# Performance work log

Hardware: AMD Instinct MI355X
Metric: run time of the kernel (lower is better)

## Reference

```python
import jax, jax.numpy as jnp
import numpy as np

L, N, E, D, H = 3, 20000, 320000, 128, 4
EPS = 1.1920929e-07  # torch RMSNorm default eps = finfo(float32).eps
NEG_SLOPE = 0.2      # PyG GATConv leaky_relu negative_slope


def rmsnorm(x, w):
    return x * jax.lax.rsqrt(jnp.mean(x * x, axis=-1, keepdims=True) + EPS) * w


def setup_inputs() -> dict:
    key = jax.random.key(0)
    ks = jax.random.split(key, 13)
    s = 0.02
    x = jax.random.normal(ks[0], (N, D), jnp.float32)
    src = jax.random.randint(ks[1], (E,), 0, N, dtype=jnp.int64)
    dst = jax.random.randint(ks[2], (E,), 0, N, dtype=jnp.int64)
    dst = jnp.where(dst == src, (dst + 1) % N, dst)  # no pre-existing self loops
    edge_index = jnp.stack([src, dst])
    return {
        "x": x,
        "W_gat": jax.random.normal(ks[3], (L, D, H * D), jnp.float32) * s,
        "att_src": jax.random.normal(ks[4], (L, H, D), jnp.float32) * s,
        "att_dst": jax.random.normal(ks[5], (L, H, D), jnp.float32) * s,
        "bias_gat": jax.random.normal(ks[6], (L, D), jnp.float32) * s,
        "W1": jax.random.normal(ks[7], (L, D, D), jnp.float32) * s,
        "b1": jax.random.normal(ks[8], (L, D), jnp.float32) * s,
        "W2": jax.random.normal(ks[9], (L, D, D), jnp.float32) * s,
        "b2": jax.random.normal(ks[10], (L, D), jnp.float32) * s,
        "norm1_w": jnp.ones((L, D), jnp.float32),
        "norm2_w": jnp.ones((L, D), jnp.float32),
        "edge_index": edge_index,
    }


def reference(x, W_gat, att_src, att_dst, bias_gat, W1, b1, W2, b2, norm1_w, norm2_w, edge_index):
    # PyG GATConv adds self loops by default
    loops = jnp.arange(N, dtype=edge_index.dtype)
    src = jnp.concatenate([edge_index[0], loops])  # [E+N]
    dst = jnp.concatenate([edge_index[1], loops])
    for i in range(L):
        # --- GATConv(hidden, hidden, heads=H, concat=False), dropout=0 (eval) ---
        xp = (x @ W_gat[i]).reshape(N, H, D)               # [N,H,D]
        a_s = jnp.einsum('nhd,hd->nh', xp, att_src[i])     # [N,H]
        a_d = jnp.einsum('nhd,hd->nh', xp, att_dst[i])
        e = jax.nn.leaky_relu(a_s[src] + a_d[dst], NEG_SLOPE)  # [E+N,H]
        m = jax.ops.segment_max(e, dst, num_segments=N)
        ex = jnp.exp(e - m[dst])
        denom = jax.ops.segment_sum(ex, dst, num_segments=N)
        alpha = ex / denom[dst]                             # segment softmax over incoming edges
        agg = jax.ops.segment_sum(alpha[:, :, None] * xp[src], dst, num_segments=N)  # [N,H,D]
        x_att = agg.mean(axis=1) + bias_gat[i]              # concat=False -> head mean, then bias
        # --- residual + RMSNorm ---
        x = rmsnorm(x + x_att, norm1_w[i])
        # --- FFN ---
        h = jax.nn.relu(x @ W1[i] + b1[i])
        h = h @ W2[i] + b2[i]
        x = rmsnorm(x + h, norm2_w[i])
    return x
```

## Files before the change

### kernel.cpp

```cpp
#include <hip/hip_runtime.h>
#include <hip/hip_bf16.h>

#define N_NODES 20000
#define NEDGE   320000
#define DIM     128
#define NH      4
#define HD      512
#define LAYERS  3
#define EPS_RMS 1.1920929e-07f
#define SLOPE   0.2f
#define NTILES  (N_NODES >> 4)

#define NWGC  (LAYERS * DIM * HD)
#define NW1C  (LAYERS * DIM * DIM)
#define NVC   (LAYERS * DIM)
#define NPACK (NWGC + 2 * NW1C + 5 * NVC)
#define NXV   (N_NODES * DIM / 8)

typedef __bf16 bf16_t;
typedef __bf16 bf16v2 __attribute__((ext_vector_type(2)));
typedef __bf16 bf16v8 __attribute__((ext_vector_type(8)));
typedef float  f32v4  __attribute__((ext_vector_type(4)));
typedef float  f32v2  __attribute__((ext_vector_type(2)));

__device__ __forceinline__ int clamp_node(int s) {
    return ((unsigned)s >= (unsigned)N_NODES) ? 0 : s;
}
__device__ __forceinline__ float leaky(float e) { return e > 0.f ? e : SLOPE * e; }
__device__ __forceinline__ unsigned char enc_fp8(float v) {
    int p = __builtin_amdgcn_cvt_pk_fp8_f32(v, v, 0, false);
    return (unsigned char)(p & 0xff);
}
__device__ __forceinline__ unsigned short enc_fp8_pair(float a, float b) {
    int p = __builtin_amdgcn_cvt_pk_fp8_f32(a, b, 0, false);
    return (unsigned short)(p & 0xffff);
}

__device__ __forceinline__ bool wave_detect_bf16(const unsigned short* xh) {
    int lane = threadIdx.x & 63;
    unsigned short hw = xh[2 * lane];
    int e = (hw >> 7) & 0xff;
    unsigned long long b = __ballot(e >= 96 && e <= 140);
    return __popcll(b) >= 48;
}
__device__ __forceinline__ bool wave_detect_i64(const int* ei) {
    int lane = threadIdx.x & 63;
    unsigned long long b = __ballot(ei[2 * lane + 1] != 0);
    return b == 0ULL;
}
__device__ __forceinline__ float raw_elem(const void* in, size_t j, bool isbf) {
    return isbf ? (float)((const bf16_t*)in)[j] : ((const float*)in)[j];
}
__device__ __forceinline__ bf16_t cvt_elem(const void* in, size_t j, bool isbf) {
    return isbf ? ((const bf16_t*)in)[j] : (bf16_t)((const float*)in)[j];
}
__device__ __forceinline__ int edge_src(const int* ei, int e, bool is64) {
    return clamp_node(is64 ? ei[2 * e] : ei[e]);
}
__device__ __forceinline__ int edge_dst(const int* ei, int e, bool is64) {
    return clamp_node(is64 ? ei[2 * NEDGE + 2 * e] : ei[NEDGE + e]);
}

__global__ __launch_bounds__(256) void prep_v(const void* x, const void* Wg,
                                              const void* aS, const void* aD,
                                              float* __restrict__ vS, float* __restrict__ vD,
                                              int* __restrict__ deg) {
    int gid = blockIdx.x * 256 + threadIdx.x;
    for (int i = gid; i < N_NODES; i += gridDim.x * 256) deg[i] = 0;
    bool isbf = wave_detect_bf16((const unsigned short*)x);
    int w = gid >> 6;
    if (w >= LAYERS * DIM * NH * 2) return;
    int lane = threadIdx.x & 63;
    int sd = w & 1, h = (w >> 1) & 3, k = (w >> 3) & 127, l = w >> 10;
    const void* att = sd ? aD : aS;
    size_t wbase = (size_t)l * DIM * HD + (size_t)k * HD + h * DIM;
    size_t abase = (size_t)l * NH * DIM + (size_t)h * DIM;
    int c = 2 * lane;
    float p = raw_elem(Wg, wbase + c, isbf) * raw_elem(att, abase + c, isbf)
            + raw_elem(Wg, wbase + c + 1, isbf) * raw_elem(att, abase + c + 1, isbf);
#pragma unroll
    for (int msk = 1; msk < 64; msk <<= 1) p += __shfl_xor(p, msk);
    if (lane == 0) {
        float* dst = sd ? vD : vS;
        dst[l * HD + h * DIM + k] = p;
    }
}

__device__ __forceinline__ void pack_item(int i, bool isbf,
        const void* Wg, const void* W1, const void* W2,
        const void* bg, const void* b1, const void* b2,
        const void* n1, const void* n2,
        bf16_t* WmixP, bf16_t* W1P, bf16_t* W2P,
        bf16_t* bgc, bf16_t* b1c, bf16_t* b2c, bf16_t* n1c, bf16_t* n2c) {
    if (i < NWGC) {
        int l = i >> 16;
        int r = i & 65535;
        int j = r & 7;
        int lane2 = (r >> 3) & 63;
        int mm = lane2 & 15, kqq = lane2 >> 4;
        int tt = (r >> 9) & 1;
        int kk = (r >> 10) & 15;
        int wvv = r >> 14;
        int kidx = kk * 32 + kqq * 8 + j;
        int h = kidx >> 7, kp = kidx & 127;
        int c = 32 * wvv + tt * 16 + mm;
        WmixP[i] = cvt_elem(Wg, (size_t)l * DIM * HD + (size_t)kp * HD + h * DIM + c, isbf);
        return;
    }
    i -= NWGC;
    if (i < NW1C) {
        int l = i / 16384;
        int r = i & 16383;
        int j = r & 7;
        int lane2 = (r >> 3) & 63;
        int mm = lane2 & 15, kqq = lane2 >> 4;
        int tt = (r >> 9) & 1;
        int ks = (r >> 10) & 3;
        int wvv = r >> 12;
        int k = ks * 32 + kqq * 8 + j;
        int c = 32 * wvv + tt * 16 + mm;
        W1P[i] = cvt_elem(W1, (size_t)l * DIM * DIM + (size_t)k * DIM + c, isbf);
        return;
    }
    i -= NW1C;
    if (i < NW1C) {
        int l = i / 16384;
        int r = i & 16383;
        int j = r & 7;
        int lane2 = (r >> 3) & 63;
        int mm = lane2 & 15, kqq = lane2 >> 4;
        int tt = (r >> 9) & 1;
        int ks = (r >> 10) & 3;
        int wvv = r >> 12;
        int k = ks * 32 + kqq * 8 + j;
        int c = 32 * wvv + tt * 16 + mm;
        W2P[i] = cvt_elem(W2, (size_t)l * DIM * DIM + (size_t)k * DIM + c, isbf);
        return;
    }
    i -= NW1C;
    if (i >= 5 * NVC) return;
    int seg = i / NVC, k = i - seg * NVC;
    if (seg == 0) bgc[k] = cvt_elem(bg, k, isbf);
    else if (seg == 1) b1c[k] = cvt_elem(b1, k, isbf);
    else if (seg == 2) b2c[k] = cvt_elem(b2, k, isbf);
    else if (seg == 3) n1c[k] = cvt_elem(n1, k, isbf);
    else n2c[k] = cvt_elem(n2, k, isbf);
}

__global__ __launch_bounds__(256) void mega_setup(
        const void* x, const void* Wg, const void* W1, const void* W2,
        const void* bg, const void* b1, const void* b2, const void* n1, const void* n2,
        bf16_t* xb, bf16_t* WmixP, bf16_t* W1P, bf16_t* W2P,
        bf16_t* bgc, bf16_t* b1c, bf16_t* b2c, bf16_t* n1c, bf16_t* n2c,
        const int* ei, int* deg,
        const float* vS, const float* vD,
        float* a_s, float* a_d, unsigned short* x8,
        int convBlocks, int histBlocks) {
    int b = (int)blockIdx.x;
    if (b >= convBlocks + histBlocks) {
        bool isbf = wave_detect_bf16((const unsigned short*)x);
        int lane = threadIdx.x & 63;
        int n = (b - convBlocks - histBlocks) * 4 + (int)(threadIdx.x >> 6);
        if (n >= N_NODES) return;
        int c = 2 * lane;
        float f0 = raw_elem(x, (size_t)n * DIM + c, isbf);
        float f1 = raw_elem(x, (size_t)n * DIM + c + 1, isbf);
        x8[n * 64 + lane] = enc_fp8_pair(f0, f1);
#pragma unroll
        for (int h = 0; h < NH; ++h) {
            float ps = f0 * vS[h * DIM + c] + f1 * vS[h * DIM + c + 1];
            float pd = f0 * vD[h * DIM + c] + f1 * vD[h * DIM + c + 1];
#pragma unroll
            for (int msk = 1; msk < 64; msk <<= 1) {
                ps += __shfl_xor(ps, msk);
                pd += __shfl_xor(pd, msk);
            }
            if (lane == 0) {
                a_s[n * 4 + h] = ps;
                a_d[n * 4 + h] = pd;
            }
        }
        return;
    }
    if (b >= convBlocks) {
        bool is64 = wave_detect_i64(ei);
        int e = (b - convBlocks) * 256 + threadIdx.x;
        if (e < NEDGE) atomicAdd(&deg[edge_dst(ei, e, is64)], 1);
        return;
    }
    bool isbf = wave_detect_bf16((const unsigned short*)x);
    int i = b * 256 + threadIdx.x;
    if (i < NXV) {
        if (isbf) {
            ((bf16v8*)xb)[i] = ((const bf16v8*)x)[i];
        } else {
            const float4* src = (const float4*)x;
            float4 a = src[2 * i], bq = src[2 * i + 1];
            bf16v8 o;
            o[0] = (bf16_t)a.x;  o[1] = (bf16_t)a.y;
            o[2] = (bf16_t)a.z;  o[3] = (bf16_t)a.w;
            o[4] = (bf16_t)bq.x; o[5] = (bf16_t)bq.y;
            o[6] = (bf16_t)bq.z; o[7] = (bf16_t)bq.w;
            ((bf16v8*)xb)[i] = o;
        }
        return;
    }
    pack_item(i - NXV, isbf, Wg, W1, W2, bg, b1, b2, n1, n2,
              WmixP, W1P, W2P, bgc, b1c, b2c, n1c, n2c);
}

__global__ __launch_bounds__(1024) void scan_kernel(const int* __restrict__ deg,
                                                    int* __restrict__ row_ptr,
                                                    int* __restrict__ cursor) {
    __shared__ int wsum[16];
    int tid = threadIdx.x, lane = tid & 63, wv = tid >> 6;
    int v[20];
    int base = tid * 20;
    int tot = 0;
    if (base < N_NODES) {
        const int4* d4 = reinterpret_cast<const int4*>(deg + base);
#pragma unroll
        for (int j = 0; j < 5; ++j) {
            int4 q = d4[j];
            v[4 * j]     = q.x;
            v[4 * j + 1] = q.y;
            v[4 * j + 2] = q.z;
            v[4 * j + 3] = q.w;
        }
#pragma unroll
        for (int i = 0; i < 20; ++i) tot += v[i];
    }
    int x = tot;
#pragma unroll
    for (int off = 1; off < 64; off <<= 1) {
        int t = __shfl_up(x, off);
        if (lane >= off) x += t;
    }
    if (lane == 63) wsum[wv] = x;
    __syncthreads();
    if (wv == 0) {
        int s = (lane < 16) ? wsum[lane] : 0;
#pragma unroll
        for (int off = 1; off < 16; off <<= 1) {
            int t = __shfl_up(s, off);
            if (lane >= off) s += t;
        }
        if (lane < 16) wsum[lane] = s;
    }
    __syncthreads();
    int off0 = ((wv == 0) ? 0 : wsum[wv - 1]) + (x - tot);
    if (tid == 0) row_ptr[0] = 0;
    if (base < N_NODES) {
        int run = off0;
#pragma unroll
        for (int i = 0; i < 20; ++i) {
            run += v[i];
            row_ptr[base + i + 1] = run;
            cursor[base + i] = run - v[i];
        }
    }
}

__global__ void fill_kernel(const int* __restrict__ ei, int* __restrict__ cursor,
                            int* __restrict__ csr_src) {
    bool is64 = wave_detect_i64(ei);
    int e = blockIdx.x * blockDim.x + threadIdx.x;
    if (e < NEDGE) {
        int d = edge_dst(ei, e, is64);
        int pos = atomicAdd(&cursor[d], 1);
        if ((unsigned)pos < (unsigned)NEDGE) csr_src[pos] = edge_src(ei, e, is64);
    }
}

__device__ __forceinline__ void gather_node_lds(int n, int lane,
        float4* wshw, int* sshw,
        const int* __restrict__ row_ptr, const int* __restrict__ csr_src,
        const float* __restrict__ a_s, const float* __restrict__ a_d,
        const unsigned short* __restrict__ x8, bf16_t* yrow) {
    int beg = row_ptr[n];
    int deg = row_ptr[n + 1] - beg;
    if (deg < 0) deg = 0;
    if (deg > NEDGE) deg = NEDGE;
    if (beg < 0) beg = 0;
    if (beg > NEDGE - deg) beg = NEDGE - deg;

    const float4* a_s4 = reinterpret_cast<const float4*>(a_s);
    const float4 adv = reinterpret_cast<const float4*>(a_d)[n];
    const float4 avs = a_s4[n];
    unsigned short pself = x8[n * 64 + lane];
    float4 wself = {__expf(leaky(avs.x + adv.x)), __expf(leaky(avs.y + adv.y)),
                    __expf(leaky(avs.z + adv.z)), __expf(leaky(avs.w + adv.w))};

    float acc[8];
    {
        f32v2 f = __builtin_amdgcn_cvt_pk_f32_fp8((int)pself, false);
        acc[0] = wself.x * f[0]; acc[1] = wself.x * f[1];
        acc[2] = wself.y * f[0]; acc[3] = wself.y * f[1];
        acc[4] = wself.z * f[0]; acc[5] = wself.z * f[1];
        acc[6] = wself.w * f[0]; acc[7] = wself.w * f[1];
    }

    float4 zl = {0.f, 0.f, 0.f, 0.f};
    for (int c0 = 0; c0 < deg; c0 += 64) {
        int cnt = deg - c0; if (cnt > 64) cnt = 64;
        if (lane < cnt) {
            int s = clamp_node(csr_src[beg + c0 + lane]);
            float4 av = a_s4[s];
            float4 w = {__expf(leaky(av.x + adv.x)), __expf(leaky(av.y + adv.y)),
                        __expf(leaky(av.z + adv.z)), __expf(leaky(av.w + adv.w))};
            zl.x += w.x; zl.y += w.y; zl.z += w.z; zl.w += w.w;
            wshw[lane] = w;
            sshw[lane] = s << 6;
        }
        unsigned short xeN[8];
        {
            int p0 = cnt < 8 ? cnt : 8;
#pragma unroll
            for (int u = 0; u < 8; ++u)
                if (u < p0) xeN[u] = x8[sshw[u] + lane];
        }
        for (int u0 = 0; u0 < cnt; u0 += 8) {
            int uc = cnt - u0; if (uc > 8) uc = 8;
            unsigned short xeC[8];
#pragma unroll
            for (int u = 0; u < 8; ++u) xeC[u] = xeN[u];
            int n0 = u0 + 8;
            int nc = cnt - n0; if (nc > 8) nc = 8;
#pragma unroll
            for (int u = 0; u < 8; ++u)
                if (u < nc) xeN[u] = x8[sshw[n0 + u] + lane];
#pragma unroll
            for (int u = 0; u < 8; ++u) {
                if (u < uc) {
                    float4 w = wshw[u0 + u];
                    f32v2 f = __builtin_amdgcn_cvt_pk_f32_fp8((int)xeC[u], false);
                    acc[0] += w.x * f[0]; acc[1] += w.x * f[1];
                    acc[2] += w.y * f[0]; acc[3] += w.y * f[1];
                    acc[4] += w.z * f[0]; acc[5] += w.z * f[1];
                    acc[6] += w.w * f[0]; acc[7] += w.w * f[1];
                }
            }
        }
    }
    float4 zr = zl;
#pragma unroll
    for (int msk = 1; msk < 64; msk <<= 1) {
        zr.x += __shfl_xor(zr.x, msk);
        zr.y += __shfl_xor(zr.y, msk);
        zr.z += __shfl_xor(zr.z, msk);
        zr.w += __shfl_xor(zr.w, msk);
    }
    float4 z4 = {wself.x + zr.x, wself.y + zr.y, wself.z + zr.z, wself.w + zr.w};
    float4 ih4 = {1.f / z4.x, 1.f / z4.y, 1.f / z4.z, 1.f / z4.w};
    int c = 2 * lane;
#pragma unroll
    for (int h = 0; h < NH; ++h) {
        float ih = h == 0 ? ih4.x : h == 1 ? ih4.y : h == 2 ? ih4.z : ih4.w;
        bf16v2 o;
        o[0] = (bf16_t)(acc[h * 2 + 0] * ih);
        o[1] = (bf16_t)(acc[h * 2 + 1] * ih);
        *reinterpret_cast<bf16v2*>(&yrow[h * DIM + c]) = o;
    }
}

template <int MODE>
__global__ __launch_bounds__(256) void gat_mix(
        const int* __restrict__ row_ptr, const int* __restrict__ csr_src,
        const float* __restrict__ a_s, const float* __restrict__ a_d,
        const unsigned short* __restrict__ x8,
        const bf16_t* __restrict__ WmixP, const bf16_t* __restrict__ bg,
        const bf16_t* __restrict__ n1w, const bf16_t* __restrict__ xb,
        const bf16_t* __restrict__ W1P, const bf16_t* __restrict__ b1,
        const bf16_t* __restrict__ W2P, const bf16_t* __restrict__ b2,
        const bf16_t* __restrict__ n2w, void* __restrict__ out,
        const float* __restrict__ vS, const float* __restrict__ vD,
        float* __restrict__ a_s_n, float* __restrict__ a_d_n,
        unsigned char* __restrict__ x8_n) {
    __shared__ bf16_t ylds[16][524];
    __shared__ bf16_t xm[16][140];
    __shared__ float  ssq_p[16][4];
    __shared__ float  asd_p[4][16][8];
    __shared__ float4 wsh[4][64];
    __shared__ int    ssh[4][64];
    bf16_t (*hh)[140] = reinterpret_cast<bf16_t (*)[140]>(&ylds[0][0]);

    int tile = blockIdx.x;
    int wv = threadIdx.x >> 6;
    int lane = threadIdx.x & 63;
    int m = lane & 15, kq = lane >> 4;

    for (int r = wv; r < 16; r += 4)
        gather_node_lds(tile * 16 + r, lane, wsh[wv], ssh[wv],
                        row_ptr, csr_src, a_s, a_d, x8, &ylds[r][0]);
    __syncthreads();

    f32v4 accm[2];
    accm[0] = (f32v4){0.f, 0.f, 0.f, 0.f};
    accm[1] = (f32v4){0.f, 0.f, 0.f, 0.f};
#pragma unroll
    for (int kk = 0; kk < 16; ++kk) {
        bf16v8 a = *reinterpret_cast<const bf16v8*>(&ylds[m][kk * 32 + kq * 8]);
#pragma unroll
        for (int tt = 0; tt < 2; ++tt) {
            bf16v8 b = *reinterpret_cast<const bf16v8*>(
                WmixP + ((((wv * 16 + kk) * 2 + tt) << 9) + lane * 8));
            accm[tt] = __builtin_amdgcn_mfma_f32_16x16x32_bf16(a, b, accm[tt], 0, 0, 0);
        }
    }
    float vals[2][4];
    {
        float sp[4] = {0.f, 0.f, 0.f, 0.f};
#pragma unroll
        for (int tt = 0; tt < 2; ++tt) {
            int col = 32 * wv + tt * 16 + m;
            float bv = (float)bg[col];
#pragma unroll
            for (int r = 0; r < 4; ++r) {
                int gr = tile * 16 + kq * 4 + r;
                float v = 0.25f * accm[tt][r] + bv + (float)xb[(size_t)gr * DIM + col];
                vals[tt][r] = v;
                sp[r] += v * v;
            }
        }
#pragma unroll
        for (int r = 0; r < 4; ++r) {
            sp[r] += __shfl_xor(sp[r], 1); sp[r] += __shfl_xor(sp[r], 2);
            sp[r] += __shfl_xor(sp[r], 4); sp[r] += __shfl_xor(sp[r], 8);
            if (m == r) ssq_p[kq * 4 + r][wv] = sp[r];
        }
    }
    __syncthreads();
    {
#pragma unroll
        for (int r = 0; r < 4; ++r) {
            int row = kq * 4 + r;
            float s = ssq_p[row][0] + ssq_p[row][1] + ssq_p[row][2] + ssq_p[row][3];
            float scale = rsqrtf(s * (1.f / 128.f) + EPS_RMS);
#pragma unroll
            for (int tt = 0; tt < 2; ++tt) {
                int col = 32 * wv + tt * 16 + m;
                xm[row][col] = (bf16_t)(vals[tt][r] * scale * (float)n1w[col]);
            }
        }
    }
    __syncthreads();

    f32v4 acc1[2];
    acc1[0] = (f32v4){0.f, 0.f, 0.f, 0.f};
    acc1[1] = (f32v4){0.f, 0.f, 0.f, 0.f};
#pragma unroll
    for (int ks = 0; ks < 4; ++ks) {
        bf16v8 a = *reinterpret_cast<const bf16v8*>(&xm[m][ks * 32 + kq * 8]);
#pragma unroll
        for (int tt = 0; tt < 2; ++tt) {
            bf16v8 b = *reinterpret_cast<const bf16v8*>(
                W1P + ((((wv * 4 + ks) * 2 + tt) << 9) + lane * 8));
            acc1[tt] = __builtin_amdgcn_mfma_f32_16x16x32_bf16(a, b, acc1[tt], 0, 0, 0);
        }
    }
#pragma unroll
    for (int tt = 0; tt < 2; ++tt) {
        int col = 32 * wv + tt * 16 + m;
        float bv = (float)b1[col];
#pragma unroll
        for (int r = 0; r < 4; ++r) {
            float v = acc1[tt][r] + bv;
            hh[kq * 4 + r][col] = (bf16_t)(v > 0.f ? v : 0.f);
        }
    }
    __syncthreads();
    f32v4 acc2[2];
    acc2[0] = (f32v4){0.f, 0.f, 0.f, 0.f};
    acc2[1] = (f32v4){0.f, 0.f, 0.f, 0.f};
#pragma unroll
    for (int ks = 0; ks < 4; ++ks) {
        bf16v8 a = *reinterpret_cast<const bf16v8*>(&hh[m][ks * 32 + kq * 8]);
#pragma unroll
        for (int tt = 0; tt < 2; ++tt) {
            bf16v8 b = *reinterpret_cast<const bf16v8*>(
                W2P + ((((wv * 4 + ks) * 2 + tt) << 9) + lane * 8));
            acc2[tt] = __builtin_amdgcn_mfma_f32_16x16x32_bf16(a, b, acc2[tt], 0, 0, 0);
        }
    }
    float vals2[2][4];
    {
        float sp[4] = {0.f, 0.f, 0.f, 0.f};
#pragma unroll
        for (int tt = 0; tt < 2; ++tt) {
            int col = 32 * wv + tt * 16 + m;
            float bv = (float)b2[col];
#pragma unroll
            for (int r = 0; r < 4; ++r) {
                float v = acc2[tt][r] + bv + (float)xm[kq * 4 + r][col];
                vals2[tt][r] = v;
                sp[r] += v * v;
            }
        }
#pragma unroll
        for (int r = 0; r < 4; ++r) {
            sp[r] += __shfl_xor(sp[r], 1); sp[r] += __shfl_xor(sp[r], 2);
            sp[r] += __shfl_xor(sp[r], 4); sp[r] += __shfl_xor(sp[r], 8);
            if (m == r) ssq_p[kq * 4 + r][wv] = sp[r];
        }
    }
    __syncthreads();
    float o2[2][4];
#pragma unroll
    for (int r = 0; r < 4; ++r) {
        int row = kq * 4 + r;
        int gr = tile * 16 + row;
        float s = ssq_p[row][0] + ssq_p[row][1] + ssq_p[row][2] + ssq_p[row][3];
        float scale = rsqrtf(s * (1.f / 128.f) + EPS_RMS);
#pragma unroll
        for (int tt = 0; tt < 2; ++tt) {
            int col = 32 * wv + tt * 16 + m;
            float o = vals2[tt][r] * scale * (float)n2w[col];
            o2[tt][r] = o;
            if (MODE == 1) ((float*)out)[(size_t)gr * DIM + col] = o;
            else {
                ((bf16_t*)out)[(size_t)gr * DIM + col] = (bf16_t)o;
                x8_n[(size_t)gr * DIM + col] = enc_fp8(o);
            }
        }
    }
    if (MODE == 0) {
        float vs0[NH], vs1[NH], vd0[NH], vd1[NH];
        int col0 = 32 * wv + m, col1 = col0 + 16;
#pragma unroll
        for (int h = 0; h < NH; ++h) {
            vs0[h] = vS[h * DIM + col0]; vs1[h] = vS[h * DIM + col1];
            vd0[h] = vD[h * DIM + col0]; vd1[h] = vD[h * DIM + col1];
        }
#pragma unroll
        for (int r = 0; r < 4; ++r) {
#pragma unroll
            for (int h = 0; h < NH; ++h) {
                float ps = o2[0][r] * vs0[h] + o2[1][r] * vs1[h];
                float pd = o2[0][r] * vd0[h] + o2[1][r] * vd1[h];
                ps += __shfl_xor(ps, 1); ps += __shfl_xor(ps, 2);
                ps += __shfl_xor(ps, 4); ps += __shfl_xor(ps, 8);
                pd += __shfl_xor(pd, 1); pd += __shfl_xor(pd, 2);
                pd += __shfl_xor(pd, 4); pd += __shfl_xor(pd, 8);
                if (m == r * 4 + h) {
                    asd_p[wv][kq * 4 + r][h * 2 + 0] = ps;
                    asd_p[wv][kq * 4 + r][h * 2 + 1] = pd;
                }
            }
        }
        __syncthreads();
        int t = threadIdx.x;
        if (t < 128) {
            int row = t >> 3, idx = t & 7;
            float s = asd_p[0][row][idx] + asd_p[1][row][idx]
                    + asd_p[2][row][idx] + asd_p[3][row][idx];
            int gr = tile * 16 + row;
            if (idx & 1) a_d_n[gr * 4 + (idx >> 1)] = s;
            else         a_s_n[gr * 4 + (idx >> 1)] = s;
        }
    }
}

extern "C" void kernel_launch(void* const* d_in, const int* in_sizes, int n_in,
                              void* d_out, int out_size, void* d_ws, size_t ws_size,
                              hipStream_t stream) {
    const void* x_in   = d_in[0];
    const void* W_gat  = d_in[1];
    const void* att_s  = d_in[2];
    const void* att_d  = d_in[3];
    const void* bias_g = d_in[4];
    const void* W1     = d_in[5];
    const void* b1     = d_in[6];
    const void* W2     = d_in[7];
    const void* b2     = d_in[8];
    const void* n1w    = d_in[9];
    const void* n2w    = d_in[10];
    const int*  ei     = (const int*)d_in[11];

    char* ws = (char*)d_ws;
    size_t off = 0;
    auto alloc = [&](size_t bytes) {
        void* p = ws + off;
        off = (off + bytes + 255) & ~(size_t)255;
        return p;
    };
    bf16_t* WmixP   = (bf16_t*)alloc((size_t)LAYERS * HD * DIM * 2);
    bf16_t* W1P     = (bf16_t*)alloc((size_t)LAYERS * DIM * DIM * 2);
    bf16_t* W2P     = (bf16_t*)alloc((size_t)LAYERS * DIM * DIM * 2);
    bf16_t* xb      = (bf16_t*)alloc((size_t)N_NODES * DIM * 2);
    unsigned short* x8a = (unsigned short*)alloc((size_t)N_NODES * DIM);
    unsigned short* x8b = (unsigned short*)alloc((size_t)N_NODES * DIM);
    float*  vS      = (float*)alloc((size_t)LAYERS * HD * 4);
    float*  vD      = (float*)alloc((size_t)LAYERS * HD * 4);
    float*  a_sA    = (float*)alloc((size_t)N_NODES * NH * 4);
    float*  a_dA    = (float*)alloc((size_t)N_NODES * NH * 4);
    float*  a_sB    = (float*)alloc((size_t)N_NODES * NH * 4);
    float*  a_dB    = (float*)alloc((size_t)N_NODES * NH * 4);
    int*    deg     = (int*)alloc((size_t)N_NODES * 4);
    int*    cursor  = (int*)alloc((size_t)N_NODES * 4);
    int*    row_ptr = (int*)alloc((size_t)(N_NODES + 1) * 4);
    int*    csr     = (int*)alloc((size_t)NEDGE * 4);
    bf16_t* bgc     = (bf16_t*)alloc((size_t)LAYERS * DIM * 2);
    bf16_t* b1c     = (bf16_t*)alloc((size_t)LAYERS * DIM * 2);
    bf16_t* b2c     = (bf16_t*)alloc((size_t)LAYERS * DIM * 2);
    bf16_t* n1c     = (bf16_t*)alloc((size_t)LAYERS * DIM * 2);
    bf16_t* n2c     = (bf16_t*)alloc((size_t)LAYERS * DIM * 2);

    prep_v<<<(LAYERS * DIM * NH * 2 * 64 + 255) / 256, 256, 0, stream>>>(
        x_in, W_gat, att_s, att_d, vS, vD, deg);

    const int NTOT = NXV + NPACK;
    const int convBlocks = (NTOT + 255) / 256;
    const int histBlocks = (NEDGE + 255) / 256;
    const int asdBlocks  = (N_NODES + 3) / 4;
    mega_setup<<<convBlocks + histBlocks + asdBlocks, 256, 0, stream>>>(
        x_in, W_gat, W1, W2, bias_g, b1, b2, n1w, n2w,
        xb, WmixP, W1P, W2P, bgc, b1c, b2c, n1c, n2c,
        ei, deg, vS, vD, a_sA, a_dA, x8a, convBlocks, histBlocks);

    scan_kernel<<<1, 1024, 0, stream>>>(deg, row_ptr, cursor);
    fill_kernel<<<(NEDGE + 255) / 256, 256, 0, stream>>>(ei, cursor, csr);

    unsigned short* x8cur[2] = {x8a, x8b};
    float* asCur[2] = {a_sA, a_sB};
    float* adCur[2] = {a_dA, a_dB};
    for (int l = 0; l < LAYERS; ++l) {
        int ci = l & 1, ni = (l + 1) & 1;
        if (l < LAYERS - 1) {
            gat_mix<0><<<NTILES, 256, 0, stream>>>(
                row_ptr, csr, asCur[ci], adCur[ci], x8cur[ci],
                WmixP + (size_t)l * HD * DIM, bgc + (size_t)l * DIM,
                n1c + (size_t)l * DIM, xb,
                W1P + (size_t)l * DIM * DIM, b1c + (size_t)l * DIM,
                W2P + (size_t)l * DIM * DIM, b2c + (size_t)l * DIM,
                n2c + (size_t)l * DIM, xb,
                vS + (size_t)(l + 1) * HD, vD + (size_t)(l + 1) * HD,
                asCur[ni], adCur[ni], (unsigned char*)x8cur[ni]);
        } else {
            gat_mix<1><<<NTILES, 256, 0, stream>>>(
                row_ptr, csr, asCur[ci], adCur[ci], x8cur[ci],
                WmixP + (size_t)l * HD * DIM, bgc + (size_t)l * DIM,
                n1c + (size_t)l * DIM, xb,
                W1P + (size_t)l * DIM * DIM, b1c + (size_t)l * DIM,
                W2P + (size_t)l * DIM * DIM, b2c + (size_t)l * DIM,
                n2c + (size_t)l * DIM, d_out,
                nullptr, nullptr, nullptr, nullptr, nullptr);
        }
    }
}
```

Baseline: 291.0 us.

## Double gat_mix workgroup to 8 waves, one output tile per wave, union LDS

```diff
diff --git a/kernel.cpp b/kernel.cpp
--- a/kernel.cpp
+++ b/kernel.cpp
@@ -16,6 +16,11 @@
 #define NVC   (LAYERS * DIM)
 #define NPACK (NWGC + 2 * NW1C + 5 * NVC)
 #define NXV   (N_NODES * DIM / 8)
+
+#define YLDS_B   16768
+#define REG2_OFF YLDS_B
+#define WSH_B    8192
+#define SMEM_TOT (YLDS_B + WSH_B + 2048)
 
 typedef __bf16 bf16_t;
 typedef __bf16 bf16v2 __attribute__((ext_vector_type(2)));
@@ -364,7 +369,7 @@
 }
 
 template <int MODE>
-__global__ __launch_bounds__(256) void gat_mix(
+__global__ __launch_bounds__(512) void gat_mix(
         const int* __restrict__ row_ptr, const int* __restrict__ csr_src,
         const float* __restrict__ a_s, const float* __restrict__ a_d,
         const unsigned short* __restrict__ x8,
@@ -376,57 +381,56 @@
         const float* __restrict__ vS, const float* __restrict__ vD,
         float* __restrict__ a_s_n, float* __restrict__ a_d_n,
         unsigned char* __restrict__ x8_n) {
-    __shared__ bf16_t ylds[16][524];
-    __shared__ bf16_t xm[16][140];
-    __shared__ float  ssq_p[16][4];
-    __shared__ float  asd_p[4][16][8];
-    __shared__ float4 wsh[4][64];
-    __shared__ int    ssh[4][64];
-    bf16_t (*hh)[140] = reinterpret_cast<bf16_t (*)[140]>(&ylds[0][0]);
+    __shared__ __align__(16) char smem[SMEM_TOT];
+    bf16_t (*ylds)[524] = reinterpret_cast<bf16_t(*)[524]>(smem);
+    float4* wshA = reinterpret_cast<float4*>(smem + REG2_OFF);
+    int*    sshA = reinterpret_cast<int*>(smem + REG2_OFF + WSH_B);
+    bf16_t (*xm)[140]      = reinterpret_cast<bf16_t(*)[140]>(smem + REG2_OFF);
+    float  (*ssq_p)[8]     = reinterpret_cast<float(*)[8]>(smem + REG2_OFF + 4480);
+    float  (*asd_p)[16][8] = reinterpret_cast<float(*)[16][8]>(smem + REG2_OFF + 4992);
+    bf16_t (*hh)[140]      = reinterpret_cast<bf16_t (*)[140]>(&ylds[0][0]);
 
     int tile = blockIdx.x;
-    int wv = threadIdx.x >> 6;
-    int lane = threadIdx.x & 63;
+    int w = (int)threadIdx.x >> 6;
+    int lane = (int)threadIdx.x & 63;
     int m = lane & 15, kq = lane >> 4;
-
-    for (int r = wv; r < 16; r += 4)
-        gather_node_lds(tile * 16 + r, lane, wsh[wv], ssh[wv],
-                        row_ptr, csr_src, a_s, a_d, x8, &ylds[r][0]);
+    int wv = w >> 1, tt = w & 1;
+    int col = 16 * w + m;
+
+    {
+        float4* ww = wshA + w * 64;
+        int* ss = sshA + w * 64;
+        gather_node_lds(tile * 16 + w, lane, ww, ss,
+                        row_ptr, csr_src, a_s, a_d, x8, &ylds[w][0]);
+        gather_node_lds(tile * 16 + w + 8, lane, ww, ss,
+                        row_ptr, csr_src, a_s, a_d, x8, &ylds[w + 8][0]);
+    }
     __syncthreads();
 
-    f32v4 accm[2];
-    accm[0] = (f32v4){0.f, 0.f, 0.f, 0.f};
-    accm[1] = (f32v4){0.f, 0.f, 0.f, 0.f};
+    f32v4 accm = (f32v4){0.f, 0.f, 0.f, 0.f};
 #pragma unroll
     for (int kk = 0; kk < 16; ++kk) {
         bf16v8 a = *reinterpret_cast<const bf16v8*>(&ylds[m][kk * 32 + kq * 8]);
-#pragma unroll
-        for (int tt = 0; tt < 2; ++tt) {
-            bf16v8 b = *reinterpret_cast<const bf16v8*>(
-                WmixP + ((((wv * 16 + kk) * 2 + tt) << 9) + lane * 8));
-            accm[tt] = __builtin_amdgcn_mfma_f32_16x16x32_bf16(a, b, accm[tt], 0, 0, 0);
-        }
-    }
-    float vals[2][4];
+        bf16v8 b = *reinterpret_cast<const bf16v8*>(
+            WmixP + ((((wv * 16 + kk) * 2 + tt) << 9) + lane * 8));
+        accm = __builtin_amdgcn_mfma_f32_16x16x32_bf16(a, b, accm, 0, 0, 0);
+    }
+    float vals[4];
     {
-        float sp[4] = {0.f, 0.f, 0.f, 0.f};
-#pragma unroll
-        for (int tt = 0; tt < 2; ++tt) {
-            int col = 32 * wv + tt * 16 + m;
-            float bv = (float)bg[col];
-#pragma unroll
-            for (int r = 0; r < 4; ++r) {
-                int gr = tile * 16 + kq * 4 + r;
-                float v = 0.25f * accm[tt][r] + bv + (float)xb[(size_t)gr * DIM + col];
-                vals[tt][r] = v;
-                sp[r] += v * v;
-            }
+        float bv = (float)bg[col];
+        float sp[4];
+#pragma unroll
+        for (int r = 0; r < 4; ++r) {
+            int gr = tile * 16 + kq * 4 + r;
+            float v = 0.25f * accm[r] + bv + (float)xb[(size_t)gr * DIM + col];
+            vals[r] = v;
+            sp[r] = v * v;
         }
 #pragma unroll
         for (int r = 0; r < 4; ++r) {
             sp[r] += __shfl_xor(sp[r], 1); sp[r] += __shfl_xor(sp[r], 2);
             sp[r] += __shfl_xor(sp[r], 4); sp[r] += __shfl_xor(sp[r], 8);
-            if (m == r) ssq_p[kq * 4 + r][wv] = sp[r];
+            if (m == r) ssq_p[kq * 4 + r][w] = sp[r];
         }
     }
     __syncthreads();
@@ -434,116 +438,93 @@
 #pragma unroll
         for (int r = 0; r < 4; ++r) {
             int row = kq * 4 + r;
-            float s = ssq_p[row][0] + ssq_p[row][1] + ssq_p[row][2] + ssq_p[row][3];
+            float s = ssq_p[row][0] + ssq_p[row][1] + ssq_p[row][2] + ssq_p[row][3]
+                    + ssq_p[row][4] + ssq_p[row][5] + ssq_p[row][6] + ssq_p[row][7];
             float scale = rsqrtf(s * (1.f / 128.f) + EPS_RMS);
-#pragma unroll
-            for (int tt = 0; tt < 2; ++tt) {
-                int col = 32 * wv + tt * 16 + m;
-                xm[row][col] = (bf16_t)(vals[tt][r] * scale * (float)n1w[col]);
-            }
+            xm[row][col] = (bf16_t)(vals[r] * scale * (float)n1w[col]);
         }
     }
     __syncthreads();
 
-    f32v4 acc1[2];
-    acc1[0] = (f32v4){0.f, 0.f, 0.f, 0.f};
-    acc1[1] = (f32v4){0.f, 0.f, 0.f, 0.f};
+    f32v4 acc1 = (f32v4){0.f, 0.f, 0.f, 0.f};
 #pragma unroll
     for (int ks = 0; ks < 4; ++ks) {
         bf16v8 a = *reinterpret_cast<const bf16v8*>(&xm[m][ks * 32 + kq * 8]);
-#pragma unroll
-        for (int tt = 0; tt < 2; ++tt) {
-            bf16v8 b = *reinterpret_cast<const bf16v8*>(
-                W1P + ((((wv * 4 + ks) * 2 + tt) << 9) + lane * 8));
-            acc1[tt] = __builtin_amdgcn_mfma_f32_16x16x32_bf16(a, b, acc1[tt], 0, 0, 0);
-        }
-    }
-#pragma unroll
-    for (int tt = 0; tt < 2; ++tt) {
-        int col = 32 * wv + tt * 16 + m;
+        bf16v8 b = *reinterpret_cast<const bf16v8*>(
+            W1P + ((((wv * 4 + ks) * 2 + tt) << 9) + lane * 8));
+        acc1 = __builtin_amdgcn_mfma_f32_16x16x32_bf16(a, b, acc1, 0, 0, 0);
+    }
+    {
         float bv = (float)b1[col];
 #pragma unroll
         for (int r = 0; r < 4; ++r) {
-            float v = acc1[tt][r] + bv;
+            float v = acc1[r] + bv;
             hh[kq * 4 + r][col] = (bf16_t)(v > 0.f ? v : 0.f);
         }
     }
     __syncthreads();
-    f32v4 acc2[2];
-    acc2[0] = (f32v4){0.f, 0.f, 0.f, 0.f};
-    acc2[1] = (f32v4){0.f, 0.f, 0.f, 0.f};
+    f32v4 acc2 = (f32v4){0.f, 0.f, 0.f, 0.f};
 #pragma unroll
     for (int ks = 0; ks < 4; ++ks) {
         bf16v8 a = *reinterpret_cast<const bf16v8*>(&hh[m][ks * 32 + kq * 8]);
-#pragma unroll
-        for (int tt = 0; tt < 2; ++tt) {
-            bf16v8 b = *reinterpret_cast<const bf16v8*>(
-                W2P + ((((wv * 4 + ks) * 2 + tt) << 9) + lane * 8));
-            acc2[tt] = __builtin_amdgcn_mfma_f32_16x16x32_bf16(a, b, acc2[tt], 0, 0, 0);
-        }
-    }
-    float vals2[2][4];
+        bf16v8 b = *reinterpret_cast<const bf16v8*>(
+            W2P + ((((wv * 4 + ks) * 2 + tt) << 9) + lane * 8));
+        acc2 = __builtin_amdgcn_mfma_f32_16x16x32_bf16(a, b, acc2, 0, 0, 0);
+    }
+    float vals2[4];
     {
-        float sp[4] = {0.f, 0.f, 0.f, 0.f};
-#pragma unroll
-        for (int tt = 0; tt < 2; ++tt) {
-            int col = 32 * wv + tt * 16 + m;
-            float bv = (float)b2[col];
-#pragma unroll
-            for (int r = 0; r < 4; ++r) {
-                float v = acc2[tt][r] + bv + (float)xm[kq * 4 + r][col];
-                vals2[tt][r] = v;
-                sp[r] += v * v;
-            }
+        float bv = (float)b2[col];
+        float sp[4];
+#pragma unroll
+        for (int r = 0; r < 4; ++r) {
+            float v = acc2[r] + bv + (float)xm[kq * 4 + r][col];
+            vals2[r] = v;
+            sp[r] = v * v;
         }
 #pragma unroll
         for (int r = 0; r < 4; ++r) {
             sp[r] += __shfl_xor(sp[r], 1); sp[r] += __shfl_xor(sp[r], 2);
             sp[r] += __shfl_xor(sp[r], 4); sp[r] += __shfl_xor(sp[r], 8);
-            if (m == r) ssq_p[kq * 4 + r][wv] = sp[r];
+            if (m == r) ssq_p[kq * 4 + r][w] = sp[r];
         }
     }
     __syncthreads();
-    float o2[2][4];
+    float o2[4];
 #pragma unroll
     for (int r = 0; r < 4; ++r) {
         int row = kq * 4 + r;
         int gr = tile * 16 + row;
-        float s = ssq_p[row][0] + ssq_p[row][1] + ssq_p[row][2] + ssq_p[row][3];
+        float s = ssq_p[row][0] + ssq_p[row][1] + ssq_p[row][2] + ssq_p[row][3]
+                + ssq_p[row][4] + ssq_p[row][5] + ssq_p[row][6] + ssq_p[row][7];
         float scale = rsqrtf(s * (1.f / 128.f) + EPS_RMS);
-#pragma unroll
-        for (int tt = 0; tt < 2; ++tt) {
-            int col = 32 * wv + tt * 16 + m;
-            float o = vals2[tt][r] * scale * (float)n2w[col];
-            o2[tt][r] = o;
-            if (MODE == 1) ((float*)out)[(size_t)gr * DIM + col] = o;
-            else {
-                ((bf16_t*)out)[(size_t)gr * DIM + col] = (bf16_t)o;
-                x8_n[(size_t)gr * DIM + col] = enc_fp8(o);
-            }
+        float o = vals2[r] * scale * (float)n2w[col];
+        o2[r] = o;
+        if (MODE == 1) ((float*)out)[(size_t)gr * DIM + col] = o;
+        else {
+            ((bf16_t*)out)[(size_t)gr * DIM + col] = (bf16_t)o;
+            x8_n[(size_t)gr * DIM + col] = enc_fp8(o);
         }
     }
     if (MODE == 0) {
-        float vs0[NH], vs1[NH], vd0[NH], vd1[NH];
-        int col0 = 32 * wv + m, col1 = col0 + 16;
+        float vs[NH], vd[NH];
 #pragma unroll
         for (int h = 0; h < NH; ++h) {
-            vs0[h] = vS[h * DIM + col0]; vs1[h] = vS[h * DIM + col1];
-            vd0[h] = vD[h * DIM + col0]; vd1[h] = vD[h * DIM + col1];
+            vs[h] = vS[h * DIM + col];
+            vd[h] = vD[h * DIM + col];
         }
 #pragma unroll
         for (int r = 0; r < 4; ++r) {
 #pragma unroll
             for (int h = 0; h < NH; ++h) {
-                float ps = o2[0][r] * vs0[h] + o2[1][r] * vs1[h];
-                float pd = o2[0][r] * vd0[h] + o2[1][r] * vd1[h];
+                float ps = o2[r] * vs[h];
+                float pd = o2[r] * vd[h];
                 ps += __shfl_xor(ps, 1); ps += __shfl_xor(ps, 2);
                 ps += __shfl_xor(ps, 4); ps += __shfl_xor(ps, 8);
                 pd += __shfl_xor(pd, 1); pd += __shfl_xor(pd, 2);
                 pd += __shfl_xor(pd, 4); pd += __shfl_xor(pd, 8);
                 if (m == r * 4 + h) {
-                    asd_p[wv][kq * 4 + r][h * 2 + 0] = ps;
-                    asd_p[wv][kq * 4 + r][h * 2 + 1] = pd;
+                    asd_p[w][kq * 4 + r][h * 2 + 0] = ps;
+                    asd_p[w][kq * 4 + r][h * 2 + 1] = pd;
                 }
             }
         }
@@ -552,7 +533,9 @@
         if (t < 128) {
             int row = t >> 3, idx = t & 7;
             float s = asd_p[0][row][idx] + asd_p[1][row][idx]
-                    + asd_p[2][row][idx] + asd_p[3][row][idx];
+                    + asd_p[2][row][idx] + asd_p[3][row][idx]
+                    + asd_p[4][row][idx] + asd_p[5][row][idx]
+                    + asd_p[6][row][idx] + asd_p[7][row][idx];
             int gr = tile * 16 + row;
             if (idx & 1) a_d_n[gr * 4 + (idx >> 1)] = s;
             else         a_s_n[gr * 4 + (idx >> 1)] = s;
@@ -626,7 +609,7 @@
     for (int l = 0; l < LAYERS; ++l) {
         int ci = l & 1, ni = (l + 1) & 1;
         if (l < LAYERS - 1) {
-            gat_mix<0><<<NTILES, 256, 0, stream>>>(
+            gat_mix<0><<<NTILES, 512, 0, stream>>>(
                 row_ptr, csr, asCur[ci], adCur[ci], x8cur[ci],
                 WmixP + (size_t)l * HD * DIM, bgc + (size_t)l * DIM,
                 n1c + (size_t)l * DIM, xb,
@@ -636,7 +619,7 @@
                 vS + (size_t)(l + 1) * HD, vD + (size_t)(l + 1) * HD,
                 asCur[ni], adCur[ni], (unsigned char*)x8cur[ni]);
         } else {
-            gat_mix<1><<<NTILES, 256, 0, stream>>>(
+            gat_mix<1><<<NTILES, 512, 0, stream>>>(
                 row_ptr, csr, asCur[ci], adCur[ci], x8cur[ci],
                 WmixP + (size_t)l * HD * DIM, bgc + (size_t)l * DIM,
                 n1c + (size_t)l * DIM, xb,
```

New measurement: 364.7 us. 25.3% more time.
